# Kernel optimization log

Measured on AMD Instinct MI355X. Metric: run time of the kernel, lower is better.

## Reference

```python
import jax, jax.numpy as jnp
import numpy as np

B, BUFF, STK, NCOMP, HIST = 128, 64, 48, 8, 96
VOCAB, WDIM, POSN, POSD = 100000, 300, 50, 50
DEP, CAD, HAD, FC, U = 40, 50, 50, 128, 256
NOUT = 2 + 2 * DEP


def setup_inputs() -> dict:
    key = jax.random.key(0)
    ks = jax.random.split(key, 40)
    d = {}
    d['buff_word_id'] = jax.random.randint(ks[0], (B, BUFF), 0, VOCAB)
    d['buff_pos_id'] = jax.random.randint(ks[1], (B, BUFF), 0, POSN)
    d['comp_word_id'] = jax.random.randint(ks[2], (B, STK, 2 * NCOMP), 0, VOCAB)
    d['comp_pos_id'] = jax.random.randint(ks[3], (B, STK, 2 * NCOMP), 0, POSN)
    d['comp_action_id'] = jax.random.randint(ks[4], (B, STK, NCOMP), 0, 2 * DEP)
    d['comp_action_len'] = jax.random.randint(ks[5], (B, STK), 0, NCOMP + 1)
    d['history_action_id'] = jax.random.randint(ks[6], (B, HIST), 0, 3 + 4 * DEP)
    d['stack_length'] = jax.random.randint(ks[7], (B,), 1, STK + 1)
    d['buff_length'] = jax.random.randint(ks[8], (B,), 1, BUFF + 1)
    d['history_action_length'] = jax.random.randint(ks[9], (B,), 1, HIST + 1)

    def w(k, shape):
        return jax.random.normal(k, shape, jnp.float32) / np.sqrt(shape[0])

    d['p_emb'] = jax.random.normal(ks[10], (POSN, POSD), jnp.float32) * 0.1
    d['comp_a_emb'] = jax.random.normal(ks[11], (2 * DEP, CAD), jnp.float32) * 0.1
    d['hist_a_emb'] = jax.random.normal(ks[12], (3 + 4 * DEP, HAD), jnp.float32) * 0.1
    d['w_emb'] = jax.random.normal(ks[13], (VOCAB, WDIM), jnp.float32) * 0.1
    d['emb_W'] = w(ks[14], (WDIM + POSD, FC)); d['emb_b'] = jnp.zeros((FC,), jnp.float32)
    d['rec_W'] = w(ks[15], (FC + CAD + FC, FC)); d['rec_b'] = jnp.zeros((FC,), jnp.float32)
    d['sW0'] = w(ks[16], (FC + U, 4 * U)); d['sb0'] = jnp.zeros((4 * U,), jnp.float32)
    d['sW1'] = w(ks[17], (U + U, 4 * U)); d['sb1'] = jnp.zeros((4 * U,), jnp.float32)
    d['bW0'] = w(ks[18], (FC + U, 4 * U)); d['bb0'] = jnp.zeros((4 * U,), jnp.float32)
    d['bW1'] = w(ks[19], (U + U, 4 * U)); d['bb1'] = jnp.zeros((4 * U,), jnp.float32)
    d['aW0'] = w(ks[20], (HAD + U, 4 * U)); d['ab0'] = jnp.zeros((4 * U,), jnp.float32)
    d['aW1'] = w(ks[21], (U + U, 4 * U)); d['ab1'] = jnp.zeros((4 * U,), jnp.float32)
    d['fW'] = w(ks[22], (3 * U, NOUT)); d['fb'] = jnp.zeros((NOUT,), jnp.float32)
    return d


def _lstm_cell(c, h, x, W, b):
    # TF LSTMCell gate order: i, j (candidate), f, o; forget_bias = 1.0
    z = jnp.concatenate([x, h], -1) @ W + b
    i, j, f, o = jnp.split(z, 4, -1)
    c = c * jax.nn.sigmoid(f + 1.0) + jax.nn.sigmoid(i) * jnp.tanh(j)
    h = jnp.tanh(c) * jax.nn.sigmoid(o)
    return c, h


def _run_lstm2(x, lengths, W0, b0, W1, b1):
    # x: [B, T, D]; returns final (at t = length) second-layer h, like dynamic_rnn's state[1].h
    Bb, T, _ = x.shape
    u = W0.shape[1] // 4
    init = tuple(jnp.zeros((Bb, u), x.dtype) for _ in range(4))

    def step(carry, inp):
        xt, t = inp
        c0, h0, c1, h1 = carry
        nc0, nh0 = _lstm_cell(c0, h0, xt, W0, b0)
        nc1, nh1 = _lstm_cell(c1, h1, nh0, W1, b1)
        m = (t < lengths)[:, None]
        new = tuple(jnp.where(m, n, o) for n, o in zip((nc0, nh0, nc1, nh1), carry))
        return new, None

    (c0, h0, c1, h1), _ = jax.lax.scan(step, init, (x.transpose(1, 0, 2), jnp.arange(T)))
    return h1


def _compose(word_id, comp_emb, act_emb, a_len, rec_W, rec_b):
    # word_id: [2N] int, comp_emb: [2N, FC], act_emb: [N, CAD], a_len: scalar
    # Sequential dict-keyed recursive composition (dict keys are head word ids).
    N = act_emb.shape[0]
    head_ids = word_id[0::2]
    dep_ids = word_id[1::2]
    idxs = jnp.arange(N)

    def step(vals, n):
        mask_h = (head_ids == head_ids[n]) & (idxs < n)
        mask_d = (head_ids == dep_ids[n]) & (idxs < n)
        ih = jnp.max(jnp.where(mask_h, idxs, -1))
        idd = jnp.max(jnp.where(mask_d, idxs, -1))
        head_e = jnp.where(ih >= 0, vals[jnp.maximum(ih, 0)], comp_emb[2 * n])
        dep_e = jnp.where(idd >= 0, vals[jnp.maximum(idd, 0)], comp_emb[2 * n + 1])
        new = jnp.tanh(jnp.concatenate([head_e, act_emb[n], dep_e]) @ rec_W + rec_b)
        return vals.at[n].set(new), new

    vals0 = jnp.zeros((N, rec_W.shape[1]), comp_emb.dtype)
    _, news = jax.lax.scan(step, vals0, idxs)
    return jnp.where(a_len == 0, comp_emb[0], news[jnp.maximum(a_len - 1, 0)])


def reference(buff_word_id, buff_pos_id, comp_word_id, comp_pos_id, comp_action_id,
              comp_action_len, history_action_id, stack_length, buff_length,
              history_action_length, p_emb, comp_a_emb, hist_a_emb, w_emb,
              emb_W, emb_b, rec_W, rec_b, sW0, sb0, sW1, sb1, bW0, bb0, bW1, bb1,
              aW0, ab0, aW1, ab1, fW, fb):
    buff_emb = jax.nn.relu(
        jnp.concatenate([w_emb[buff_word_id], p_emb[buff_pos_id]], -1) @ emb_W + emb_b)
    comp_emb = jax.nn.relu(
        jnp.concatenate([w_emb[comp_word_id], p_emb[comp_pos_id]], -1) @ emb_W + emb_b)
    act_emb = comp_a_emb[comp_action_id]        # [B, STK, N, CAD]
    hist_emb = hist_a_emb[history_action_id]    # [B, HIST, HAD]

    comp_fn = lambda wi, ce, ae, al: _compose(wi, ce, ae, al, rec_W, rec_b)
    stack_emb = jax.vmap(jax.vmap(comp_fn))(comp_word_id, comp_emb, act_emb, comp_action_len)

    h_s = _run_lstm2(stack_emb, stack_length, sW0, sb0, sW1, sb1)
    h_b = _run_lstm2(buff_emb, buff_length, bW0, bb0, bW1, bb1)
    h_a = _run_lstm2(hist_emb, history_action_length, aW0, ab0, aW1, ab1)
    return jnp.concatenate([h_s, h_b, h_a], -1) @ fW + fb
```

## Files before the change

### kernel.cpp

```cpp
#include <hip/hip_runtime.h>

#define BB    128
#define BUFF  64
#define STK   48
#define NCOMP 8
#define HIST  96
#define WDIM  300
#define POSD  50
#define CAD   50
#define HAD   50
#define FC    128
#define UU    256
#define NOUT  82

typedef __bf16 bf16;
typedef __attribute__((ext_vector_type(8))) __bf16 bf16x8;
typedef __attribute__((ext_vector_type(4))) float   f32x4;

__device__ __forceinline__ float sigf(float x)   { return 1.f / (1.f + __expf(-x)); }
__device__ __forceinline__ float tanhf_(float x) { return 1.f - 2.f / (1.f + __expf(2.f * x)); }

__device__ __forceinline__ unsigned pack2(const float* p) {
  union { unsigned u; bf16 h[2]; } r;
  r.h[0] = (bf16)p[0]; r.h[1] = (bf16)p[1];
  return r.u;
}

__device__ __forceinline__ bf16x8 aload16(const bf16* p) {
  union { unsigned long long q[2]; bf16x8 v; } u;
  u.q[0] = __hip_atomic_load((const unsigned long long*)p,       __ATOMIC_RELAXED, __HIP_MEMORY_SCOPE_AGENT);
  u.q[1] = __hip_atomic_load((const unsigned long long*)(p + 4), __ATOMIC_RELAXED, __HIP_MEMORY_SCOPE_AGENT);
  return u.v;
}

__global__ __launch_bounds__(256) void k_emb(
    const int* bw, const int* bp, const int* cw, const int* cp,
    const float* w_emb, const float* p_emb, const float* embW, const float* embB,
    bf16* comp_emb, bf16* buff_emb)
{
  __shared__ __align__(16) char sm[138752];
  bf16*  A  = (bf16*)sm;
  bf16*  Wt = (bf16*)(sm + 46080);
  float* sb = (float*)(sm + 46080 + 92160);

  const int tid = threadIdx.x;
  const int r0  = blockIdx.x * 64;

  for (int i = tid; i < 64 * 176; i += 256) {
    int m = i / 176, c2 = i % 176, e0 = 2 * c2;
    int r = r0 + m;
    unsigned v;
    if (e0 < 300) {
      int word = (r < 98304) ? cw[r] : bw[r - 98304];
      v = pack2(w_emb + word * 300 + e0);
    } else if (e0 < 350) {
      int pos = (r < 98304) ? cp[r] : bp[r - 98304];
      v = pack2(p_emb + pos * 50 + (e0 - 300));
    } else v = 0u;
    *(unsigned*)(A + m * 360 + e0) = v;
  }
  for (int i = tid; i < 350 * 128; i += 256) {
    int k = i >> 7, n = i & 127;
    Wt[n * 360 + k] = (bf16)embW[i];
  }
  { int i = tid; if (i < 256) { int n = i >> 1; Wt[n * 360 + 350 + (i & 1)] = (bf16)0.f; } }
  if (tid < 128) sb[tid] = embB[tid];
  __syncthreads();

  const int wv = tid >> 6, lane = tid & 63, l15 = lane & 15, quad = lane >> 4;
  f32x4 acc[8];
#pragma unroll
  for (int i = 0; i < 8; ++i) acc[i] = (f32x4){0.f, 0.f, 0.f, 0.f};

  const bf16* Arow = A + (wv * 16 + l15) * 360;
  for (int ks = 0; ks < 11; ++ks) {
    int kq = ks * 32 + quad * 8;
    bf16x8 a = *(const bf16x8*)(Arow + kq);
#pragma unroll
    for (int nt = 0; nt < 8; ++nt) {
      bf16x8 b = *(const bf16x8*)(Wt + (nt * 16 + l15) * 360 + kq);
      acc[nt] = __builtin_amdgcn_mfma_f32_16x16x32_bf16(a, b, acc[nt], 0, 0, 0);
    }
  }
#pragma unroll
  for (int nt = 0; nt < 8; ++nt)
#pragma unroll
    for (int rr = 0; rr < 4; ++rr) {
      int row = wv * 16 + quad * 4 + rr;
      int n   = nt * 16 + l15;
      float z = fmaxf(acc[nt][rr] + sb[n], 0.f);
      int r = r0 + row;
      bf16 o = (bf16)z;
      if (r < 98304) comp_emb[r * 128 + n] = o;
      else           buff_emb[(r - 98304) * 128 + n] = o;
    }
}

__global__ __launch_bounds__(256) void k_compose(
    const int* cw, const int* caid, const int* calen,
    const bf16* comp_emb, const float* ca_emb, const float* recW, const float* recB,
    bf16* stack_emb)
{
  __shared__ __align__(16) char sm[129344];
  bf16*  Wt   = (bf16*)sm;
  bf16*  X    = (bf16*)(sm + 83968);
  bf16*  VALS = (bf16*)(sm + 94464);
  float* recb = (float*)(sm + 127232);
  int*   IH   = (int*)(sm + 127744);
  int*   ID   = (int*)(sm + 128256);
  int*   AN   = (int*)(sm + 128768);
  int*   ALEN = (int*)(sm + 129280);

  const int tid = threadIdx.x;
  const int bs0 = blockIdx.x * 16;

  for (int i = tid; i < 306 * 128; i += 256) {
    int k = i >> 7, n = i & 127;
    Wt[n * 328 + k] = (bf16)recW[i];
  }
  for (int i = tid; i < 128 * 22; i += 256) {
    int n = i / 22, k = 306 + i % 22;
    Wt[n * 328 + k] = (bf16)0.f;
  }
  if (tid < 128) recb[tid] = recB[tid];
  if (tid < 16) {
    int bs = bs0 + tid;
    int hid[8], did[8];
#pragma unroll
    for (int m = 0; m < 8; ++m) { hid[m] = cw[bs * 16 + 2 * m]; did[m] = cw[bs * 16 + 2 * m + 1]; }
    for (int n = 0; n < 8; ++n) {
      int ih = -1, idd = -1;
      for (int m = 0; m < n; ++m) { if (hid[m] == hid[n]) ih = m; if (hid[m] == did[n]) idd = m; }
      IH[tid * 8 + n] = ih; ID[tid * 8 + n] = idd; AN[tid * 8 + n] = caid[bs * 8 + n];
    }
    ALEN[tid] = calen[bs];
  }
  __syncthreads();

  const int wv = tid >> 6, lane = tid & 63, l15 = lane & 15, quad = lane >> 4;

  for (int n = 0; n < 8; ++n) {
    for (int i = tid; i < 16 * 160; i += 256) {
      int p = i / 160, c2 = i % 160, e0 = 2 * c2;
      int bs = bs0 + p;
      unsigned v;
      if (e0 < 128) {
        int ih = IH[p * 8 + n];
        v = (ih >= 0) ? *(const unsigned*)(VALS + (p * 8 + ih) * 128 + e0)
                      : *(const unsigned*)(comp_emb + (bs * 16 + 2 * n) * 128 + e0);
      } else if (e0 < 178) {
        v = pack2(ca_emb + AN[p * 8 + n] * 50 + (e0 - 128));
      } else if (e0 < 306) {
        int e = e0 - 178;
        int idd = ID[p * 8 + n];
        v = (idd >= 0) ? *(const unsigned*)(VALS + (p * 8 + idd) * 128 + e)
                       : *(const unsigned*)(comp_emb + (bs * 16 + 2 * n + 1) * 128 + e);
      } else v = 0u;
      *(unsigned*)(X + p * 328 + e0) = v;
    }
    __syncthreads();

    f32x4 acc[2];
    acc[0] = (f32x4){0.f,0.f,0.f,0.f}; acc[1] = (f32x4){0.f,0.f,0.f,0.f};
    for (int ks = 0; ks < 10; ++ks) {
      int kq = ks * 32 + quad * 8;
      bf16x8 a = *(const bf16x8*)(X + l15 * 328 + kq);
#pragma unroll
      for (int t2 = 0; t2 < 2; ++t2) {
        int nt = 2 * wv + t2;
        bf16x8 b = *(const bf16x8*)(Wt + (nt * 16 + l15) * 328 + kq);
        acc[t2] = __builtin_amdgcn_mfma_f32_16x16x32_bf16(a, b, acc[t2], 0, 0, 0);
      }
    }
    __syncthreads();
#pragma unroll
    for (int t2 = 0; t2 < 2; ++t2) {
      int nt = 2 * wv + t2;
#pragma unroll
      for (int rr = 0; rr < 4; ++rr) {
        int p = quad * 4 + rr;
        int col = nt * 16 + l15;
        VALS[(p * 8 + n) * 128 + col] = (bf16)tanhf_(acc[t2][rr] + recb[col]);
      }
    }
    __syncthreads();
  }

  for (int i = tid; i < 16 * 64; i += 256) {
    int p = i / 64, c2 = i % 64, e0 = 2 * c2;
    int bs = bs0 + p;
    int al = ALEN[p];
    unsigned v = (al == 0) ? *(const unsigned*)(comp_emb + (bs * 16) * 128 + e0)
                           : *(const unsigned*)(VALS + (p * 8 + (al - 1)) * 128 + e0);
    *(unsigned*)(stack_emb + bs * 128 + e0) = v;
  }
}

struct BarT { int cnt; int pad[31]; };

__global__ __launch_bounds__(256) void k_lstm(
    const float* sW0, const float* sb0, const float* sW1, const float* sb1,
    const float* bW0, const float* bb0, const float* bW1, const float* bb1,
    const float* aW0, const float* ab0, const float* aW1, const float* ab1,
    const bf16* stack_emb, const bf16* buff_emb, const float* hist_tab, const int* hist_id,
    const int* len_s, const int* len_b, const int* len_a,
    bf16* h0buf, bf16* h1buf, BarT* bars)
{
  __shared__ __align__(16) char sm[143872];
  const int tid = threadIdx.x;
  const int bx  = blockIdx.x;
  const int L     = bx >> 4;
  const int rid   = bx & 15;
  const int layer = rid >> 3;
  const int u0    = (rid & 7) * 32;
  const int T     = (L == 0) ? STK : (L == 1) ? BUFF : HIST;
  const int* lenp = (L == 0) ? len_s : (L == 1) ? len_b : len_a;

  const float *W, *bias;
  int K, KP, Kxp;
  if (layer == 0) {
    W = (L == 0) ? sW0 : (L == 1) ? bW0 : aW0;
    bias = (L == 0) ? sb0 : (L == 1) ? bb0 : ab0;
    if (L == 2) { K = 320; KP = 328; Kxp = 64; } else { K = 384; KP = 392; Kxp = 128; }
  } else {
    W = (L == 0) ? sW1 : (L == 1) ? bW1 : aW1;
    bias = (L == 0) ? sb1 : (L == 1) ? bb1 : ab1;
    K = 512; KP = 520; Kxp = 256;
  }
  bf16*  Wt     = (bf16*)sm;
  bf16*  hstage = (bf16*)(sm + 128 * KP * 2);
  float* sb     = (float*)(sm + 128 * KP * 2 + 9216);
  bf16*  Xa     = (bf16*)(sm + 128 * KP * 2 + 9216 + 512);

  for (int i = tid; i < K * 128; i += 256) {
    int kk = i >> 7, cc = i & 127;
    int col = (cc >> 5) * 256 + u0 + (cc & 31);
    bf16 v;
    if (layer == 0 && L == 2) {
      if (kk < 64) v = (kk < 50) ? (bf16)W[kk * 1024 + col] : (bf16)0.f;
      else         v = (bf16)W[(kk - 14) * 1024 + col];
    } else v = (bf16)W[kk * 1024 + col];
    Wt[cc * KP + kk] = v;
  }
  if (tid < 128) { int col = (tid >> 5) * 256 + u0 + (tid & 31); sb[tid] = bias[col]; }

  const int wv = tid >> 6, lane = tid & 63, l15 = lane & 15, quad = lane >> 4;
  int lenr[8];
#pragma unroll
  for (int mt = 0; mt < 2; ++mt)
#pragma unroll
    for (int rr = 0; rr < 4; ++rr)
      lenr[mt * 4 + rr] = lenp[32 * wv + 16 * mt + quad * 4 + rr];

  float cst[16], hst[16];
#pragma unroll
  for (int i = 0; i < 16; ++i) { cst[i] = 0.f; hst[i] = 0.f; }

  BarT* bar = bars + L;
  bf16* h0w = h0buf + L * 2 * 32768;
  bf16* h1w = h1buf + L * 2 * 32768;
  const bf16* xsrc = (L == 0) ? stack_emb : buff_emb;
  const int Tx = (L == 0) ? STK : BUFF;

  __syncthreads();

  for (int p = 0; p <= T; ++p) {
    const bool active = (layer == 0) ? (p < T) : (p >= 1);
    const int  t = (layer == 0) ? p : (p - 1);

    if (L == 2 && layer == 0 && active) {
      for (int i = tid; i < 128 * 32; i += 256) {
        int row = i >> 5, e0 = 2 * (i & 31);
        unsigned v = 0u;
        if (e0 < 50) { int id = hist_id[row * 96 + t]; v = pack2(hist_tab + id * 50 + e0); }
        *(unsigned*)(Xa + row * 72 + e0) = v;
      }
    }
    __syncthreads();

    if (active) {
      f32x4 acc[2][8];
#pragma unroll
      for (int a1 = 0; a1 < 2; ++a1)
#pragma unroll
        for (int a2 = 0; a2 < 8; ++a2) acc[a1][a2] = (f32x4){0.f, 0.f, 0.f, 0.f};

      const bf16* h0r = h0w + ((p - 1) & 1) * 32768;
      const bf16* h1r = h1w + (p & 1) * 32768;

      for (int ks = 0; ks < K / 32; ++ks) {
        int k0 = ks * 32;
        int kq = k0 + quad * 8;
        bf16x8 a[2];
#pragma unroll
        for (int mt = 0; mt < 2; ++mt) {
          int row = 32 * wv + 16 * mt + l15;
          if (layer == 0) {
            if (k0 < Kxp) {
              if (L == 2) a[mt] = *(const bf16x8*)(Xa + row * 72 + kq);
              else        a[mt] = *(const bf16x8*)(xsrc + (row * Tx + t) * 128 + kq);
            } else a[mt] = aload16(h0r + row * 256 + (kq - Kxp));
          } else {
            if (k0 < 256) a[mt] = aload16(h0r + row * 256 + kq);
            else          a[mt] = aload16(h1r + row * 256 + (kq - 256));
          }
        }
#pragma unroll
        for (int nt = 0; nt < 8; ++nt) {
          bf16x8 b = *(const bf16x8*)(Wt + (nt * 16 + l15) * KP + kq);
          acc[0][nt] = __builtin_amdgcn_mfma_f32_16x16x32_bf16(a[0], b, acc[0][nt], 0, 0, 0);
          acc[1][nt] = __builtin_amdgcn_mfma_f32_16x16x32_bf16(a[1], b, acc[1][nt], 0, 0, 0);
        }
      }
#pragma unroll
      for (int mt = 0; mt < 2; ++mt)
#pragma unroll
        for (int g2 = 0; g2 < 2; ++g2)
#pragma unroll
          for (int rr = 0; rr < 4; ++rr) {
            int row = 32 * wv + 16 * mt + quad * 4 + rr;
            float zi = acc[mt][0 + g2][rr] + sb[(0 + g2) * 16 + l15];
            float zj = acc[mt][2 + g2][rr] + sb[(2 + g2) * 16 + l15];
            float zf = acc[mt][4 + g2][rr] + sb[(4 + g2) * 16 + l15];
            float zo = acc[mt][6 + g2][rr] + sb[(6 + g2) * 16 + l15];
            float ig = sigf(zi), jg = tanhf_(zj), fg = sigf(zf + 1.f), og = sigf(zo);
            int idx = mt * 8 + g2 * 4 + rr;
            float cn = cst[idx] * fg + ig * jg;
            float hn = tanhf_(cn) * og;
            bool mk = (t < lenr[mt * 4 + rr]);
            cst[idx] = mk ? cn : cst[idx];
            hst[idx] = mk ? hn : hst[idx];
            hstage[row * 36 + g2 * 16 + l15] = (bf16)hst[idx];
          }
    }
    __syncthreads();
    if (active) {
      bf16* dst = (layer == 0) ? (h0w + (p & 1) * 32768) : (h1w + ((p - 1) & 1) * 32768);
      for (int i = tid; i < 128 * 8; i += 256) {
        int row = i >> 3, c = i & 7;
        unsigned long long v = *(const unsigned long long*)(hstage + row * 36 + c * 4);
        __hip_atomic_store((unsigned long long*)(dst + row * 256 + u0 + c * 4), v,
                           __ATOMIC_RELAXED, __HIP_MEMORY_SCOPE_AGENT);
      }
    }
    __syncthreads();
    if (tid == 0) {
      __builtin_amdgcn_sched_barrier(0);
      const int target = 16 * (p + 1);
      int prev = __hip_atomic_fetch_add(&bar->cnt, 1, __ATOMIC_RELAXED, __HIP_MEMORY_SCOPE_AGENT);
      if (prev != target - 1) {
        while (__hip_atomic_load(&bar->cnt, __ATOMIC_RELAXED, __HIP_MEMORY_SCOPE_AGENT) < target) { }
      }
      __builtin_amdgcn_sched_barrier(0);
    }
    __syncthreads();
  }
}

__global__ __launch_bounds__(128) void k_final(
    const bf16* h1buf, const float* fW, const float* fb, float* out)
{
  __shared__ float hs[768];
  const int b = blockIdx.x, tid = threadIdx.x;
  for (int i = tid; i < 768; i += 128) {
    int L = i >> 8, u = i & 255;
    hs[i] = (float)h1buf[(L * 2 + 1) * 32768 + b * 256 + u];
  }
  __syncthreads();
  if (tid < NOUT) {
    float acc = fb[tid];
    for (int u = 0; u < 768; ++u) acc += hs[u] * fW[u * NOUT + tid];
    out[b * NOUT + tid] = acc;
  }
}

extern "C" void kernel_launch(void* const* d_in, const int* in_sizes, int n_in,
                              void* d_out, int out_size, void* d_ws, size_t ws_size,
                              hipStream_t stream)
{
  (void)in_sizes; (void)n_in; (void)out_size; (void)ws_size;
  char* ws = (char*)d_ws;
  BarT* bars      = (BarT*)ws;
  bf16* h0buf     = (bf16*)(ws + 512);
  bf16* h1buf     = (bf16*)(ws + 512 + 393216);
  bf16* comp_emb  = (bf16*)(ws + 786944);
  bf16* buff_emb  = (bf16*)(ws + 786944 + 25165824);
  bf16* stack_emb = (bf16*)(ws + 786944 + 25165824 + 2097152);

  hipMemsetAsync(ws, 0, 786944, stream);

  k_emb<<<1664, 256, 0, stream>>>(
      (const int*)d_in[0], (const int*)d_in[1], (const int*)d_in[2], (const int*)d_in[3],
      (const float*)d_in[13], (const float*)d_in[10], (const float*)d_in[14], (const float*)d_in[15],
      comp_emb, buff_emb);

  k_compose<<<384, 256, 0, stream>>>(
      (const int*)d_in[2], (const int*)d_in[4], (const int*)d_in[5],
      comp_emb, (const float*)d_in[11], (const float*)d_in[16], (const float*)d_in[17],
      stack_emb);

  k_lstm<<<48, 256, 0, stream>>>(
      (const float*)d_in[18], (const float*)d_in[19], (const float*)d_in[20], (const float*)d_in[21],
      (const float*)d_in[22], (const float*)d_in[23], (const float*)d_in[24], (const float*)d_in[25],
      (const float*)d_in[26], (const float*)d_in[27], (const float*)d_in[28], (const float*)d_in[29],
      stack_emb, buff_emb, (const float*)d_in[12], (const int*)d_in[6],
      (const int*)d_in[7], (const int*)d_in[8], (const int*)d_in[9],
      h0buf, h1buf, bars);

  k_final<<<128, 128, 0, stream>>>(h1buf, (const float*)d_in[30], (const float*)d_in[31],
                                   (float*)d_out);
}
```

Baseline: 2.110 ms.

## Split LSTM by batch slices per block, removing cross-block grid barriers

Replaces the 48-block LSTM kernel, which split gate columns across blocks and synchronised every timestep with global atomic barriers, with a 64-block kernel in which each block owns a 16-row batch slice and runs both layers locally. The recurrent state stays in shared memory and only __syncthreads is needed. Weights are pre-transposed to bf16 by a separate prep kernel and streamed from global memory or L2 on each step instead of being held in LDS. Blocks are mapped to XCDs by sequence type. The cost is reloading the full weight matrices every step from cache, plus only 24 working blocks, with the two layers serialised inside each block instead of pipelined.

```diff
diff --git a/kernel.cpp b/kernel.cpp
--- a/kernel.cpp
+++ b/kernel.cpp
@@ -1,16 +1,8 @@
 #include <hip/hip_runtime.h>
 
-#define BB    128
 #define BUFF  64
 #define STK   48
-#define NCOMP 8
 #define HIST  96
-#define WDIM  300
-#define POSD  50
-#define CAD   50
-#define HAD   50
-#define FC    128
-#define UU    256
 #define NOUT  82
 
 typedef __bf16 bf16;
@@ -24,13 +16,6 @@
   union { unsigned u; bf16 h[2]; } r;
   r.h[0] = (bf16)p[0]; r.h[1] = (bf16)p[1];
   return r.u;
-}
-
-__device__ __forceinline__ bf16x8 aload16(const bf16* p) {
-  union { unsigned long long q[2]; bf16x8 v; } u;
-  u.q[0] = __hip_atomic_load((const unsigned long long*)p,       __ATOMIC_RELAXED, __HIP_MEMORY_SCOPE_AGENT);
-  u.q[1] = __hip_atomic_load((const unsigned long long*)(p + 4), __ATOMIC_RELAXED, __HIP_MEMORY_SCOPE_AGENT);
-  return u.v;
 }
 
 __global__ __launch_bounds__(256) void k_emb(
@@ -196,165 +181,182 @@
   }
 }
 
-struct BarT { int cnt; int pad[31]; };
-
-__global__ __launch_bounds__(256) void k_lstm(
-    const float* sW0, const float* sb0, const float* sW1, const float* sb1,
-    const float* bW0, const float* bb0, const float* bW1, const float* bb1,
-    const float* aW0, const float* ab0, const float* aW1, const float* ab1,
-    const bf16* stack_emb, const bf16* buff_emb, const float* hist_tab, const int* hist_id,
+__global__ __launch_bounds__(256) void k_wprep(
+    const float* s0, const float* b0, const float* a0,
+    const float* s1, const float* b1, const float* a1,
+    bf16* d0, bf16* d1, bf16* d2, bf16* d3, bf16* d4, bf16* d5)
+{
+  const int m = blockIdx.y;
+  const int Kd = (m == 2) ? 320 : (m < 2 ? 384 : 512);
+  const int total = 1024 * Kd;
+  int idx = blockIdx.x * 256 + threadIdx.x;
+  if (idx >= total) return;
+  int n = idx / Kd, k = idx - n * Kd;
+  const float* src = (m==0)?s0:(m==1)?b0:(m==2)?a0:(m==3)?s1:(m==4)?b1:a1;
+  bf16* dst        = (m==0)?d0:(m==1)?d1:(m==2)?d2:(m==3)?d3:(m==4)?d4:d5;
+  int ksrc = k;
+  if (m == 2) ksrc = (k < 50) ? k : (k < 64 ? -1 : k - 14);
+  float v = (ksrc >= 0) ? src[ksrc * 1024 + n] : 0.f;
+  dst[n * Kd + k] = (bf16)v;
+}
+
+__global__ __launch_bounds__(512) void k_lstm2(
+    const bf16* w0s, const bf16* w0b, const bf16* w0a,
+    const bf16* w1s, const bf16* w1b, const bf16* w1a,
+    const float* sb0, const float* sb1, const float* bb0, const float* bb1,
+    const float* ab0, const float* ab1,
+    const bf16* stack_emb, const bf16* buff_emb,
+    const float* hist_tab, const int* hist_id,
     const int* len_s, const int* len_b, const int* len_a,
-    bf16* h0buf, bf16* h1buf, BarT* bars)
-{
-  __shared__ __align__(16) char sm[143872];
+    bf16* h1out)
+{
+  const int bx = blockIdx.x;
+  const int xcd = bx & 7, r = bx >> 3;
+  int L, slice;
+  if (xcd < 3)      { L = 0; slice = r * 3 + xcd; }
+  else if (xcd < 5) { L = 1; slice = r * 2 + (xcd - 3); }
+  else              { L = 2; slice = r * 3 + (xcd - 5); }
+  if (slice >= 8) return;
+
+  const bf16* W0T  = (L == 0) ? w0s : (L == 1) ? w0b : w0a;
+  const bf16* W1T  = (L == 0) ? w1s : (L == 1) ? w1b : w1a;
+  const float* B0  = (L == 0) ? sb0 : (L == 1) ? bb0 : ab0;
+  const float* B1  = (L == 0) ? sb1 : (L == 1) ? bb1 : ab1;
+  const int* lenp  = (L == 0) ? len_s : (L == 1) ? len_b : len_a;
+  const int T      = (L == 0) ? STK : (L == 1) ? BUFF : HIST;
+  const int K0p    = (L == 2) ? 320 : 384;
+  const bf16* xsrc = (L == 0) ? stack_emb : buff_emb;
+  const int Tx     = (L == 0) ? STK : BUFF;
+
+  __shared__ __align__(16) bf16 h0s[2][16][280];
+  __shared__ __align__(16) bf16 h1s[2][16][280];
+  __shared__ __align__(16) bf16 Xa[16][88];
+
   const int tid = threadIdx.x;
-  const int bx  = blockIdx.x;
-  const int L     = bx >> 4;
-  const int rid   = bx & 15;
-  const int layer = rid >> 3;
-  const int u0    = (rid & 7) * 32;
-  const int T     = (L == 0) ? STK : (L == 1) ? BUFF : HIST;
-  const int* lenp = (L == 0) ? len_s : (L == 1) ? len_b : len_a;
-
-  const float *W, *bias;
-  int K, KP, Kxp;
-  if (layer == 0) {
-    W = (L == 0) ? sW0 : (L == 1) ? bW0 : aW0;
-    bias = (L == 0) ? sb0 : (L == 1) ? bb0 : ab0;
-    if (L == 2) { K = 320; KP = 328; Kxp = 64; } else { K = 384; KP = 392; Kxp = 128; }
-  } else {
-    W = (L == 0) ? sW1 : (L == 1) ? bW1 : aW1;
-    bias = (L == 0) ? sb1 : (L == 1) ? bb1 : ab1;
-    K = 512; KP = 520; Kxp = 256;
-  }
-  bf16*  Wt     = (bf16*)sm;
-  bf16*  hstage = (bf16*)(sm + 128 * KP * 2);
-  float* sb     = (float*)(sm + 128 * KP * 2 + 9216);
-  bf16*  Xa     = (bf16*)(sm + 128 * KP * 2 + 9216 + 512);
-
-  for (int i = tid; i < K * 128; i += 256) {
-    int kk = i >> 7, cc = i & 127;
-    int col = (cc >> 5) * 256 + u0 + (cc & 31);
-    bf16 v;
-    if (layer == 0 && L == 2) {
-      if (kk < 64) v = (kk < 50) ? (bf16)W[kk * 1024 + col] : (bf16)0.f;
-      else         v = (bf16)W[(kk - 14) * 1024 + col];
-    } else v = (bf16)W[kk * 1024 + col];
-    Wt[cc * KP + kk] = v;
-  }
-  if (tid < 128) { int col = (tid >> 5) * 256 + u0 + (tid & 31); sb[tid] = bias[col]; }
-
   const int wv = tid >> 6, lane = tid & 63, l15 = lane & 15, quad = lane >> 4;
-  int lenr[8];
-#pragma unroll
-  for (int mt = 0; mt < 2; ++mt)
+
+  for (int i = tid; i < 2 * 16 * 280; i += 512) {
+    ((bf16*)h0s)[i] = (bf16)0.f;
+    ((bf16*)h1s)[i] = (bf16)0.f;
+  }
+
+  float bia0[8], bia1[8];
+#pragma unroll
+  for (int nt = 0; nt < 8; ++nt) {
+    int col = (nt >> 1) * 256 + wv * 32 + (nt & 1) * 16 + l15;
+    bia0[nt] = B0[col]; bia1[nt] = B1[col];
+  }
+  int lenr[4];
+#pragma unroll
+  for (int rr = 0; rr < 4; ++rr) lenr[rr] = lenp[slice * 16 + quad * 4 + rr];
+
+  float c0[8], h0v[8], c1[8], h1v[8];
+#pragma unroll
+  for (int i = 0; i < 8; ++i) { c0[i] = h0v[i] = c1[i] = h1v[i] = 0.f; }
+
+  for (int t = 0; t < T; ++t) {
+    const int pt = t & 1, pr = pt ^ 1;
+
+    if (L == 2) {
+      int row = tid >> 5, e0 = (tid & 31) * 2;
+      int id = hist_id[(slice * 16 + row) * HIST + t];
+      unsigned v = 0u;
+      if (e0 < 50) v = pack2(hist_tab + id * 50 + e0);
+      *(unsigned*)(&Xa[row][e0]) = v;
+    }
+    __syncthreads();
+
+    f32x4 acc[8];
+#pragma unroll
+    for (int i = 0; i < 8; ++i) acc[i] = (f32x4){0.f, 0.f, 0.f, 0.f};
+
+    if (L == 2) {
+#pragma unroll
+      for (int ks = 0; ks < 10; ++ks) {
+        int kq = ks * 32 + quad * 8;
+        bf16x8 a = (ks < 2) ? *(const bf16x8*)(&Xa[l15][kq])
+                            : *(const bf16x8*)(&h0s[pr][l15][kq - 64]);
+#pragma unroll
+        for (int nt = 0; nt < 8; ++nt) {
+          int n0 = (nt >> 1) * 256 + wv * 32 + (nt & 1) * 16;
+          bf16x8 b = *(const bf16x8*)(W0T + (n0 + l15) * 320 + kq);
+          acc[nt] = __builtin_amdgcn_mfma_f32_16x16x32_bf16(a, b, acc[nt], 0, 0, 0);
+        }
+      }
+    } else {
+#pragma unroll
+      for (int ks = 0; ks < 12; ++ks) {
+        int kq = ks * 32 + quad * 8;
+        bf16x8 a = (ks < 4)
+          ? *(const bf16x8*)(xsrc + ((slice * 16 + l15) * Tx + t) * 128 + kq)
+          : *(const bf16x8*)(&h0s[pr][l15][kq - 128]);
+#pragma unroll
+        for (int nt = 0; nt < 8; ++nt) {
+          int n0 = (nt >> 1) * 256 + wv * 32 + (nt & 1) * 16;
+          bf16x8 b = *(const bf16x8*)(W0T + (n0 + l15) * 384 + kq);
+          acc[nt] = __builtin_amdgcn_mfma_f32_16x16x32_bf16(a, b, acc[nt], 0, 0, 0);
+        }
+      }
+    }
+#pragma unroll
+    for (int t16 = 0; t16 < 2; ++t16)
+#pragma unroll
+      for (int rr = 0; rr < 4; ++rr) {
+        float zi = acc[0 + t16][rr] + bia0[0 + t16];
+        float zj = acc[2 + t16][rr] + bia0[2 + t16];
+        float zf = acc[4 + t16][rr] + bia0[4 + t16];
+        float zo = acc[6 + t16][rr] + bia0[6 + t16];
+        float ig = sigf(zi), jg = tanhf_(zj), fg = sigf(zf + 1.f), og = sigf(zo);
+        int idx = t16 * 4 + rr;
+        float cn = c0[idx] * fg + ig * jg;
+        float hn = tanhf_(cn) * og;
+        bool mk = (t < lenr[rr]);
+        c0[idx]  = mk ? cn : c0[idx];
+        h0v[idx] = mk ? hn : h0v[idx];
+        h0s[pt][quad * 4 + rr][wv * 32 + t16 * 16 + l15] = (bf16)h0v[idx];
+      }
+    __syncthreads();
+
+#pragma unroll
+    for (int i = 0; i < 8; ++i) acc[i] = (f32x4){0.f, 0.f, 0.f, 0.f};
+#pragma unroll
+    for (int ks = 0; ks < 16; ++ks) {
+      int kq = ks * 32 + quad * 8;
+      bf16x8 a = (ks < 8) ? *(const bf16x8*)(&h0s[pt][l15][kq])
+                          : *(const bf16x8*)(&h1s[pr][l15][kq - 256]);
+#pragma unroll
+      for (int nt = 0; nt < 8; ++nt) {
+        int n0 = (nt >> 1) * 256 + wv * 32 + (nt & 1) * 16;
+        bf16x8 b = *(const bf16x8*)(W1T + (n0 + l15) * 512 + kq);
+        acc[nt] = __builtin_amdgcn_mfma_f32_16x16x32_bf16(a, b, acc[nt], 0, 0, 0);
+      }
+    }
+#pragma unroll
+    for (int t16 = 0; t16 < 2; ++t16)
+#pragma unroll
+      for (int rr = 0; rr < 4; ++rr) {
+        float zi = acc[0 + t16][rr] + bia1[0 + t16];
+        float zj = acc[2 + t16][rr] + bia1[2 + t16];
+        float zf = acc[4 + t16][rr] + bia1[4 + t16];
+        float zo = acc[6 + t16][rr] + bia1[6 + t16];
+        float ig = sigf(zi), jg = tanhf_(zj), fg = sigf(zf + 1.f), og = sigf(zo);
+        int idx = t16 * 4 + rr;
+        float cn = c1[idx] * fg + ig * jg;
+        float hn = tanhf_(cn) * og;
+        bool mk = (t < lenr[rr]);
+        c1[idx]  = mk ? cn : c1[idx];
+        h1v[idx] = mk ? hn : h1v[idx];
+        h1s[pt][quad * 4 + rr][wv * 32 + t16 * 16 + l15] = (bf16)h1v[idx];
+      }
+    __syncthreads();
+  }
+
+#pragma unroll
+  for (int t16 = 0; t16 < 2; ++t16)
 #pragma unroll
     for (int rr = 0; rr < 4; ++rr)
-      lenr[mt * 4 + rr] = lenp[32 * wv + 16 * mt + quad * 4 + rr];
-
-  float cst[16], hst[16];
-#pragma unroll
-  for (int i = 0; i < 16; ++i) { cst[i] = 0.f; hst[i] = 0.f; }
-
-  BarT* bar = bars + L;
-  bf16* h0w = h0buf + L * 2 * 32768;
-  bf16* h1w = h1buf + L * 2 * 32768;
-  const bf16* xsrc = (L == 0) ? stack_emb : buff_emb;
-  const int Tx = (L == 0) ? STK : BUFF;
-
-  __syncthreads();
-
-  for (int p = 0; p <= T; ++p) {
-    const bool active = (layer == 0) ? (p < T) : (p >= 1);
-    const int  t = (layer == 0) ? p : (p - 1);
-
-    if (L == 2 && layer == 0 && active) {
-      for (int i = tid; i < 128 * 32; i += 256) {
-        int row = i >> 5, e0 = 2 * (i & 31);
-        unsigned v = 0u;
-        if (e0 < 50) { int id = hist_id[row * 96 + t]; v = pack2(hist_tab + id * 50 + e0); }
-        *(unsigned*)(Xa + row * 72 + e0) = v;
-      }
-    }
-    __syncthreads();
-
-    if (active) {
-      f32x4 acc[2][8];
-#pragma unroll
-      for (int a1 = 0; a1 < 2; ++a1)
-#pragma unroll
-        for (int a2 = 0; a2 < 8; ++a2) acc[a1][a2] = (f32x4){0.f, 0.f, 0.f, 0.f};
-
-      const bf16* h0r = h0w + ((p - 1) & 1) * 32768;
-      const bf16* h1r = h1w + (p & 1) * 32768;
-
-      for (int ks = 0; ks < K / 32; ++ks) {
-        int k0 = ks * 32;
-        int kq = k0 + quad * 8;
-        bf16x8 a[2];
-#pragma unroll
-        for (int mt = 0; mt < 2; ++mt) {
-          int row = 32 * wv + 16 * mt + l15;
-          if (layer == 0) {
-            if (k0 < Kxp) {
-              if (L == 2) a[mt] = *(const bf16x8*)(Xa + row * 72 + kq);
-              else        a[mt] = *(const bf16x8*)(xsrc + (row * Tx + t) * 128 + kq);
-            } else a[mt] = aload16(h0r + row * 256 + (kq - Kxp));
-          } else {
-            if (k0 < 256) a[mt] = aload16(h0r + row * 256 + kq);
-            else          a[mt] = aload16(h1r + row * 256 + (kq - 256));
-          }
-        }
-#pragma unroll
-        for (int nt = 0; nt < 8; ++nt) {
-          bf16x8 b = *(const bf16x8*)(Wt + (nt * 16 + l15) * KP + kq);
-          acc[0][nt] = __builtin_amdgcn_mfma_f32_16x16x32_bf16(a[0], b, acc[0][nt], 0, 0, 0);
-          acc[1][nt] = __builtin_amdgcn_mfma_f32_16x16x32_bf16(a[1], b, acc[1][nt], 0, 0, 0);
-        }
-      }
-#pragma unroll
-      for (int mt = 0; mt < 2; ++mt)
-#pragma unroll
-        for (int g2 = 0; g2 < 2; ++g2)
-#pragma unroll
-          for (int rr = 0; rr < 4; ++rr) {
-            int row = 32 * wv + 16 * mt + quad * 4 + rr;
-            float zi = acc[mt][0 + g2][rr] + sb[(0 + g2) * 16 + l15];
-            float zj = acc[mt][2 + g2][rr] + sb[(2 + g2) * 16 + l15];
-            float zf = acc[mt][4 + g2][rr] + sb[(4 + g2) * 16 + l15];
-            float zo = acc[mt][6 + g2][rr] + sb[(6 + g2) * 16 + l15];
-            float ig = sigf(zi), jg = tanhf_(zj), fg = sigf(zf + 1.f), og = sigf(zo);
-            int idx = mt * 8 + g2 * 4 + rr;
-            float cn = cst[idx] * fg + ig * jg;
-            float hn = tanhf_(cn) * og;
-            bool mk = (t < lenr[mt * 4 + rr]);
-            cst[idx] = mk ? cn : cst[idx];
-            hst[idx] = mk ? hn : hst[idx];
-            hstage[row * 36 + g2 * 16 + l15] = (bf16)hst[idx];
-          }
-    }
-    __syncthreads();
-    if (active) {
-      bf16* dst = (layer == 0) ? (h0w + (p & 1) * 32768) : (h1w + ((p - 1) & 1) * 32768);
-      for (int i = tid; i < 128 * 8; i += 256) {
-        int row = i >> 3, c = i & 7;
-        unsigned long long v = *(const unsigned long long*)(hstage + row * 36 + c * 4);
-        __hip_atomic_store((unsigned long long*)(dst + row * 256 + u0 + c * 4), v,
-                           __ATOMIC_RELAXED, __HIP_MEMORY_SCOPE_AGENT);
-      }
-    }
-    __syncthreads();
-    if (tid == 0) {
-      __builtin_amdgcn_sched_barrier(0);
-      const int target = 16 * (p + 1);
-      int prev = __hip_atomic_fetch_add(&bar->cnt, 1, __ATOMIC_RELAXED, __HIP_MEMORY_SCOPE_AGENT);
-      if (prev != target - 1) {
-        while (__hip_atomic_load(&bar->cnt, __ATOMIC_RELAXED, __HIP_MEMORY_SCOPE_AGENT) < target) { }
-      }
-      __builtin_amdgcn_sched_barrier(0);
-    }
-    __syncthreads();
-  }
+      h1out[L * 32768 + (slice * 16 + quad * 4 + rr) * 256 + wv * 32 + t16 * 16 + l15] =
+          (bf16)h1v[t16 * 4 + rr];
 }
 
 __global__ __launch_bounds__(128) void k_final(
@@ -363,8 +365,8 @@
   __shared__ float hs[768];
   const int b = blockIdx.x, tid = threadIdx.x;
   for (int i = tid; i < 768; i += 128) {
-    int L = i >> 8, u = i & 255;
-    hs[i] = (float)h1buf[(L * 2 + 1) * 32768 + b * 256 + u];
+    int Li = i >> 8, u = i & 255;
+    hs[i] = (float)h1buf[Li * 32768 + b * 256 + u];
   }
   __syncthreads();
   if (tid < NOUT) {
@@ -380,14 +382,16 @@
 {
   (void)in_sizes; (void)n_in; (void)out_size; (void)ws_size;
   char* ws = (char*)d_ws;
-  BarT* bars      = (BarT*)ws;
-  bf16* h0buf     = (bf16*)(ws + 512);
-  bf16* h1buf     = (bf16*)(ws + 512 + 393216);
+  bf16* h1buf     = (bf16*)ws;
   bf16* comp_emb  = (bf16*)(ws + 786944);
+  bf16* wT_s0 = (bf16*)(ws + 786944);
+  bf16* wT_b0 = (bf16*)(ws + 786944 + 786432);
+  bf16* wT_a0 = (bf16*)(ws + 786944 + 1572864);
+  bf16* wT_s1 = (bf16*)(ws + 786944 + 2228224);
+  bf16* wT_b1 = (bf16*)(ws + 786944 + 3276800);
+  bf16* wT_a1 = (bf16*)(ws + 786944 + 4325376);
   bf16* buff_emb  = (bf16*)(ws + 786944 + 25165824);
   bf16* stack_emb = (bf16*)(ws + 786944 + 25165824 + 2097152);
-
-  hipMemsetAsync(ws, 0, 786944, stream);
 
   k_emb<<<1664, 256, 0, stream>>>(
       (const int*)d_in[0], (const int*)d_in[1], (const int*)d_in[2], (const int*)d_in[3],
@@ -399,13 +403,19 @@
       comp_emb, (const float*)d_in[11], (const float*)d_in[16], (const float*)d_in[17],
       stack_emb);
 
-  k_lstm<<<48, 256, 0, stream>>>(
-      (const float*)d_in[18], (const float*)d_in[19], (const float*)d_in[20], (const float*)d_in[21],
-      (const float*)d_in[22], (const float*)d_in[23], (const float*)d_in[24], (const float*)d_in[25],
-      (const float*)d_in[26], (const float*)d_in[27], (const float*)d_in[28], (const float*)d_in[29],
+  k_wprep<<<dim3(2048, 6), 256, 0, stream>>>(
+      (const float*)d_in[18], (const float*)d_in[22], (const float*)d_in[26],
+      (const float*)d_in[20], (const float*)d_in[24], (const float*)d_in[28],
+      wT_s0, wT_b0, wT_a0, wT_s1, wT_b1, wT_a1);
+
+  k_lstm2<<<64, 512, 0, stream>>>(
+      wT_s0, wT_b0, wT_a0, wT_s1, wT_b1, wT_a1,
+      (const float*)d_in[19], (const float*)d_in[21],
+      (const float*)d_in[23], (const float*)d_in[25],
+      (const float*)d_in[27], (const float*)d_in[29],
       stack_emb, buff_emb, (const float*)d_in[12], (const int*)d_in[6],
       (const int*)d_in[7], (const int*)d_in[8], (const int*)d_in[9],
-      h0buf, h1buf, bars);
+      h1buf);
 
   k_final<<<128, 128, 0, stream>>>(h1buf, (const float*)d_in[30], (const float*)d_in[31],
                                    (float*)d_out);
```

Result: slower. 5.514 ms (+161.4%).

## Pin each LSTM group to one XCC and use intra-XCC barriers

Applied to the files above, without the earlier changes.

The LSTM kernel now launches many blocks. Each block reads its hardware XCC id, and the first 16 blocks on XCCs 0 to 2 claim the roles for the stack, buffer and history LSTMs; the other blocks exit. Since every LSTM's 16 cooperating blocks now share one XCC and its L2, the per-step barrier uses workgroup-scope atomics and volatile polling, and hidden states move through volatile loads and stores instead of agent-scope atomics. This is meant to cut the per-timestep synchronisation and cross-die coherence latency that dominates the recurrence. It relies on the hardware dispatching enough blocks to each XCC and on the L2 being coherent within an XCC, and it adds wasted block launches plus a separate final-state buffer.

```diff
diff --git a/kernel.cpp b/kernel.cpp
--- a/kernel.cpp
+++ b/kernel.cpp
@@ -1,16 +1,8 @@
 #include <hip/hip_runtime.h>
 
-#define BB    128
 #define BUFF  64
 #define STK   48
-#define NCOMP 8
 #define HIST  96
-#define WDIM  300
-#define POSD  50
-#define CAD   50
-#define HAD   50
-#define FC    128
-#define UU    256
 #define NOUT  82
 
 typedef __bf16 bf16;
@@ -26,11 +18,15 @@
   return r.u;
 }
 
-__device__ __forceinline__ bf16x8 aload16(const bf16* p) {
+__device__ __forceinline__ bf16x8 vload16(const bf16* p) {
   union { unsigned long long q[2]; bf16x8 v; } u;
-  u.q[0] = __hip_atomic_load((const unsigned long long*)p,       __ATOMIC_RELAXED, __HIP_MEMORY_SCOPE_AGENT);
-  u.q[1] = __hip_atomic_load((const unsigned long long*)(p + 4), __ATOMIC_RELAXED, __HIP_MEMORY_SCOPE_AGENT);
+  const volatile unsigned long long* vp = (const volatile unsigned long long*)p;
+  u.q[0] = vp[0];
+  u.q[1] = vp[1];
   return u.v;
+}
+__device__ __forceinline__ void vstore8(bf16* p, unsigned long long v) {
+  *(volatile unsigned long long*)p = v;
 }
 
 __global__ __launch_bounds__(256) void k_emb(
@@ -196,21 +192,34 @@
   }
 }
 
-struct BarT { int cnt; int pad[31]; };
-
-__global__ __launch_bounds__(256) void k_lstm(
+struct __align__(256) Ctr { int cnt; int pad[63]; };
+
+__global__ __launch_bounds__(256) void k_lstm3(
     const float* sW0, const float* sb0, const float* sW1, const float* sb1,
     const float* bW0, const float* bb0, const float* bW1, const float* bb1,
     const float* aW0, const float* ab0, const float* aW1, const float* ab1,
     const bf16* stack_emb, const bf16* buff_emb, const float* hist_tab, const int* hist_id,
     const int* len_s, const int* len_b, const int* len_a,
-    bf16* h0buf, bf16* h1buf, BarT* bars)
+    bf16* h0buf, bf16* h1buf, bf16* h1out, Ctr* claims, Ctr* bars)
 {
   __shared__ __align__(16) char sm[143872];
+  __shared__ int role_sh;
   const int tid = threadIdx.x;
-  const int bx  = blockIdx.x;
-  const int L     = bx >> 4;
-  const int rid   = bx & 15;
+
+  unsigned xcc;
+  asm volatile("s_getreg_b32 %0, hwreg(HW_REG_XCC_ID)" : "=s"(xcc));
+  if (tid == 0) {
+    int rr = -1;
+    if (xcc < 3)
+      rr = __hip_atomic_fetch_add(&claims[xcc].cnt, 1, __ATOMIC_RELAXED,
+                                  __HIP_MEMORY_SCOPE_WORKGROUP);
+    role_sh = (rr >= 0 && rr < 16) ? rr : -1;
+  }
+  __syncthreads();
+  const int rid = role_sh;
+  if (rid < 0) return;
+
+  const int L     = (int)xcc;
   const int layer = rid >> 3;
   const int u0    = (rid & 7) * 32;
   const int T     = (L == 0) ? STK : (L == 1) ? BUFF : HIST;
@@ -256,7 +265,7 @@
 #pragma unroll
   for (int i = 0; i < 16; ++i) { cst[i] = 0.f; hst[i] = 0.f; }
 
-  BarT* bar = bars + L;
+  Ctr* bar = bars + L;
   bf16* h0w = h0buf + L * 2 * 32768;
   bf16* h1w = h1buf + L * 2 * 32768;
   const bf16* xsrc = (L == 0) ? stack_emb : buff_emb;
@@ -299,10 +308,10 @@
             if (k0 < Kxp) {
               if (L == 2) a[mt] = *(const bf16x8*)(Xa + row * 72 + kq);
               else        a[mt] = *(const bf16x8*)(xsrc + (row * Tx + t) * 128 + kq);
-            } else a[mt] = aload16(h0r + row * 256 + (kq - Kxp));
+            } else a[mt] = vload16(h0r + row * 256 + (kq - Kxp));
           } else {
-            if (k0 < 256) a[mt] = aload16(h0r + row * 256 + kq);
-            else          a[mt] = aload16(h1r + row * 256 + (kq - 256));
+            if (k0 < 256) a[mt] = vload16(h0r + row * 256 + kq);
+            else          a[mt] = vload16(h1r + row * 256 + (kq - 256));
           }
         }
 #pragma unroll
@@ -339,32 +348,39 @@
       for (int i = tid; i < 128 * 8; i += 256) {
         int row = i >> 3, c = i & 7;
         unsigned long long v = *(const unsigned long long*)(hstage + row * 36 + c * 4);
-        __hip_atomic_store((unsigned long long*)(dst + row * 256 + u0 + c * 4), v,
-                           __ATOMIC_RELAXED, __HIP_MEMORY_SCOPE_AGENT);
+        vstore8(dst + row * 256 + u0 + c * 4, v);
       }
     }
     __syncthreads();
     if (tid == 0) {
-      __builtin_amdgcn_sched_barrier(0);
+      __hip_atomic_fetch_add(&bar->cnt, 1, __ATOMIC_RELAXED, __HIP_MEMORY_SCOPE_WORKGROUP);
       const int target = 16 * (p + 1);
-      int prev = __hip_atomic_fetch_add(&bar->cnt, 1, __ATOMIC_RELAXED, __HIP_MEMORY_SCOPE_AGENT);
-      if (prev != target - 1) {
-        while (__hip_atomic_load(&bar->cnt, __ATOMIC_RELAXED, __HIP_MEMORY_SCOPE_AGENT) < target) { }
-      }
-      __builtin_amdgcn_sched_barrier(0);
-    }
-    __syncthreads();
+      while (*(volatile int*)&bar->cnt < target) { }
+    }
+    __syncthreads();
+  }
+
+  if (layer == 1) {
+#pragma unroll
+    for (int mt = 0; mt < 2; ++mt)
+#pragma unroll
+      for (int g2 = 0; g2 < 2; ++g2)
+#pragma unroll
+        for (int rr = 0; rr < 4; ++rr) {
+          int row = 32 * wv + 16 * mt + quad * 4 + rr;
+          h1out[L * 32768 + row * 256 + u0 + g2 * 16 + l15] = (bf16)hst[mt * 8 + g2 * 4 + rr];
+        }
   }
 }
 
 __global__ __launch_bounds__(128) void k_final(
-    const bf16* h1buf, const float* fW, const float* fb, float* out)
+    const bf16* h1out, const float* fW, const float* fb, float* out)
 {
   __shared__ float hs[768];
   const int b = blockIdx.x, tid = threadIdx.x;
   for (int i = tid; i < 768; i += 128) {
-    int L = i >> 8, u = i & 255;
-    hs[i] = (float)h1buf[(L * 2 + 1) * 32768 + b * 256 + u];
+    int Li = i >> 8, u = i & 255;
+    hs[i] = (float)h1out[Li * 32768 + b * 256 + u];
   }
   __syncthreads();
   if (tid < NOUT) {
@@ -380,9 +396,11 @@
 {
   (void)in_sizes; (void)n_in; (void)out_size; (void)ws_size;
   char* ws = (char*)d_ws;
-  BarT* bars      = (BarT*)ws;
   bf16* h0buf     = (bf16*)(ws + 512);
   bf16* h1buf     = (bf16*)(ws + 512 + 393216);
+  Ctr*  claims    = (Ctr*)(ws + 786944);
+  Ctr*  bars      = (Ctr*)(ws + 786944 + 1024);
+  bf16* h1out     = (bf16*)(ws + 786944 + 4096);
   bf16* comp_emb  = (bf16*)(ws + 786944);
   bf16* buff_emb  = (bf16*)(ws + 786944 + 25165824);
   bf16* stack_emb = (bf16*)(ws + 786944 + 25165824 + 2097152);
@@ -399,14 +417,16 @@
       comp_emb, (const float*)d_in[11], (const float*)d_in[16], (const float*)d_in[17],
       stack_emb);
 
-  k_lstm<<<48, 256, 0, stream>>>(
+  hipMemsetAsync(ws + 786944, 0, 4096, stream);
+
+  k_lstm3<<<512, 256, 0, stream>>>(
       (const float*)d_in[18], (const float*)d_in[19], (const float*)d_in[20], (const float*)d_in[21],
       (const float*)d_in[22], (const float*)d_in[23], (const float*)d_in[24], (const float*)d_in[25],
       (const float*)d_in[26], (const float*)d_in[27], (const float*)d_in[28], (const float*)d_in[29],
       stack_emb, buff_emb, (const float*)d_in[12], (const int*)d_in[6],
       (const int*)d_in[7], (const int*)d_in[8], (const int*)d_in[9],
-      h0buf, h1buf, bars);
-
-  k_final<<<128, 128, 0, stream>>>(h1buf, (const float*)d_in[30], (const float*)d_in[31],
+      h0buf, h1buf, h1out, claims, bars);
+
+  k_final<<<128, 128, 0, stream>>>(h1out, (const float*)d_in[30], (const float*)d_in[31],
                                    (float*)d_out);
 }
```

Measured after the change: 2.853 ms. 1.35x slower.
